# Kernel optimization log

Hardware: AMD Instinct MI355X
Metric: run time of the kernel (lower is better)

The kernel has to match this reference:

```python
import jax, jax.numpy as jnp
import numpy as np

N_NODES = 100000
N_EDGES = 1600000
MAX_RADIUS = 3.0
NUM_BASIS = 3
SQRT2 = 2.0 ** 0.5
# e3nn soft_one_hot_linspace 'smooth_finite' prefactor
C_SMOOTH = 1.14136 * float(np.exp(2.0))


def _sus(x):
    # smooth unit step: exp(-1/x) for x>0 else 0 (NaN-safe for grad)
    safe = jnp.where(x > 0.0, x, 1.0)
    return jnp.where(x > 0.0, jnp.exp(-1.0 / safe), 0.0)


def radial_embed(d):
    # soft_one_hot_linspace(d, 0, max_radius, 3, basis='smooth_finite', cutoff=True) * sqrt(num_basis)
    values = jnp.linspace(0.0, MAX_RADIUS, NUM_BASIS + 2)[1:-1]  # [3]
    step = MAX_RADIUS / (NUM_BASIS + 1)
    diff = (d[:, None] - values) / step  # [E,3]
    y = C_SMOOTH * _sus(diff + 1.0) * _sus(1.0 - diff)
    return y * (NUM_BASIS ** 0.5)


def fcnet(x, w1, w2):
    # e3nn FullyConnectedNet([3,16,numel], relu): normalized weights, normalize2mom(relu)=sqrt(2)*relu
    h = SQRT2 * jax.nn.relu(x @ (w1 / w1.shape[0] ** 0.5))
    return h @ (w2 / w2.shape[0] ** 0.5)


def reference(pos, feat, edge_src, edge_dst, fc1_w1, fc1_w2, core_w1, core_w2, fc3_w1, fc3_w2, conv_w, conv_b):
    n = pos.shape[0]
    z = edge_src.shape[0] / n  # average num neighbors
    edge_vec = pos[edge_dst] - pos[edge_src]
    d = jnp.sqrt(jnp.sum(edge_vec * edge_vec, axis=1))  # edges are self-loop-free -> d > 0
    emb = radial_embed(d)  # [E,3]

    # NOTE on e3nn math: with input/mid/output parities all even and sh = 0e+1o+2e,
    # the only parity-allowed paths producing nonzero output are the 0e (scalar) paths,
    # which contract against Y_0 = 1 ('component' normalization). The 4x1e block of the
    # mid irreps is identically zero (no parity-allowed path ever populates it), so the
    # math below (scalar block only, with e3nn path weights) is exactly equivalent.
    def conv(x, w1, w2, mul_in, mul_out, path_w):
        # per-edge weights from radial MLP; keep the 0e->0e instruction block
        w = fcnet(emb, w1, w2)[:, : mul_in * mul_out].reshape(-1, mul_in, mul_out)
        msg = path_w * jnp.einsum('euw,eu->ew', w, x[edge_src])
        return jax.ops.segment_sum(msg, edge_dst, num_segments=n) / z ** 0.5

    x = conv(feat, fc1_w1, fc1_w2, 3, 4, (1.0 / 3.0) ** 0.5)  # tp1: fan_in 3*1 -> pw=1/sqrt(3)
    for i in range(3):
        x = conv(x, core_w1[i], core_w2[i], 4, 4, 0.5)  # tp2 0e path: pw=sqrt(1/4)
    x = conv(x, fc3_w1, fc3_w2, 4, 16, 0.5)  # tp3: pw=sqrt(1/4)
    # Conv1d(16, 2, 1) == pointwise linear
    return x @ conv_w.T + conv_b


def setup_inputs():
    key = jax.random.key(0)
    ks = jax.random.split(key, 12)
    pos = jax.random.uniform(ks[0], (N_NODES, 3), dtype=jnp.float32)  # unit box -> all edge lengths < max_radius
    feat = jax.random.normal(ks[1], (N_NODES, 3), dtype=jnp.float32)
    edge_src = jax.random.randint(ks[2], (N_EDGES,), 0, N_NODES, dtype=jnp.int32)
    off = jax.random.randint(ks[3], (N_EDGES,), 1, N_NODES, dtype=jnp.int32)
    edge_dst = ((edge_src + off) % N_NODES).astype(jnp.int32)  # radius_graph has no self-loops
    return {
        'pos': pos,
        'feat': feat,
        'edge_src': edge_src,
        'edge_dst': edge_dst,
        'fc1_w1': jax.random.normal(ks[4], (3, 16), jnp.float32),
        'fc1_w2': jax.random.normal(ks[5], (16, 12), jnp.float32),
        'core_w1': jax.random.normal(ks[6], (3, 3, 16), jnp.float32),
        'core_w2': jax.random.normal(ks[7], (3, 16, 48), jnp.float32),
        'fc3_w1': jax.random.normal(ks[8], (3, 16), jnp.float32),
        'fc3_w2': jax.random.normal(ks[9], (16, 64), jnp.float32),
        'conv_w': jax.random.normal(ks[10], (2, 16), jnp.float32) * 0.25,
        'conv_b': jax.random.normal(ks[11], (2,), jnp.float32) * 0.1,
    }
```

## Files before the change

### kernel.cpp

```cpp
#include <hip/hip_runtime.h>


#define BCAP 4608
#define NBMAX 400

__device__ __forceinline__ float sus_f(float x) {
    return x > 0.0f ? __expf(-1.0f / x) : 0.0f;
}

__device__ __forceinline__ float uload(const float* p) {
    return __uint_as_float(__builtin_amdgcn_readfirstlane(__float_as_uint(*p)));
}

__global__ __launch_bounds__(128) void k_prep_g(
    const float* __restrict__ w2, const float* __restrict__ cw,
    float* __restrict__ gbuf)
{
    int idx = threadIdx.x;
    int k = idx >> 3, u = (idx >> 1) & 3, c = idx & 1;
    float s = 0.0f;
    #pragma unroll
    for (int w = 0; w < 16; ++w)
        s = fmaf(w2[k * 64 + u * 16 + w], cw[c * 16 + w], s);
    gbuf[idx] = s;
}

__global__ __launch_bounds__(256) void k_bin(
    const int* __restrict__ src, const int* __restrict__ dst,
    int* __restrict__ gcur, int* __restrict__ ptmp,
    int nedges, int nb)
{
    __shared__ int cnt[NBMAX];
    __shared__ int gb[NBMAX];
    for (int b = threadIdx.x; b < nb; b += 256) cnt[b] = 0;
    __syncthreads();

    int base = blockIdx.x * 2048 + threadIdx.x * 8;
    int pk[8]; int bk[8]; short r[8];
    int ss[8], dd[8];
    if (base + 7 < nedges) {
        int4 s0 = *(const int4*)&src[base];
        int4 s1 = *(const int4*)&src[base + 4];
        int4 d0 = *(const int4*)&dst[base];
        int4 d1 = *(const int4*)&dst[base + 4];
        ss[0]=s0.x; ss[1]=s0.y; ss[2]=s0.z; ss[3]=s0.w;
        ss[4]=s1.x; ss[5]=s1.y; ss[6]=s1.z; ss[7]=s1.w;
        dd[0]=d0.x; dd[1]=d0.y; dd[2]=d0.z; dd[3]=d0.w;
        dd[4]=d1.x; dd[5]=d1.y; dd[6]=d1.z; dd[7]=d1.w;
        #pragma unroll
        for (int i = 0; i < 8; ++i) {
            int b = dd[i] >> 8;
            bk[i] = b;
            pk[i] = (ss[i] << 8) | (dd[i] & 255);
            r[i] = (short)atomicAdd(&cnt[b], 1);
        }
    } else {
        #pragma unroll
        for (int i = 0; i < 8; ++i) {
            int e = base + i;
            if (e < nedges) {
                int s = src[e], t = dst[e];
                int b = t >> 8;
                bk[i] = b;
                pk[i] = (s << 8) | (t & 255);
                r[i] = (short)atomicAdd(&cnt[b], 1);
            } else bk[i] = -1;
        }
    }
    __syncthreads();
    for (int b = threadIdx.x; b < nb; b += 256) {
        int c = cnt[b];
        gb[b] = c > 0 ? atomicAdd(&gcur[b], c) : 0;
    }
    __syncthreads();
    #pragma unroll
    for (int i = 0; i < 8; ++i) {
        if (bk[i] >= 0) {
            int p = gb[bk[i]] + (int)r[i];
            if (p < BCAP)
                ptmp[bk[i] * BCAP + p] = pk[i];
        }
    }
}

__global__ __launch_bounds__(256) void k_build(
    const int* __restrict__ gcur, const int* __restrict__ ptmp,
    int* __restrict__ pidx, int2* __restrict__ offs2,
    int n, int nb)
{
    int b = blockIdx.x;
    int cnt = gcur[b]; if (cnt > BCAP) cnt = BCAP;

    __shared__ int stage[BCAP];
    __shared__ int perm[BCAP];
    __shared__ int deg[256];
    __shared__ int loffs[256];
    __shared__ int cur[256];

    const int* tin = ptmp + b * BCAP;
    for (int j = threadIdx.x; j < cnt; j += 256) stage[j] = tin[j];
    deg[threadIdx.x] = 0;
    __syncthreads();

    for (int j = threadIdx.x; j < cnt; j += 256)
        atomicAdd(&deg[stage[j] & 255], 1);
    __syncthreads();

    {
        int t = threadIdx.x;
        int v = deg[t];
        loffs[t] = v; __syncthreads();
        for (int off = 1; off < 256; off <<= 1) {
            int val = (t >= off) ? loffs[t - off] : 0;
            __syncthreads();
            loffs[t] += val;
            __syncthreads();
        }
        int incl = loffs[t];
        __syncthreads();
        loffs[t] = incl - v;
        cur[t] = incl - v;
        __syncthreads();
    }

    {
        int nid0 = b << 8;
        int nn = n - nid0; if (nn > 256) nn = 256;
        int t = threadIdx.x;
        if (t < nn) {
            int st = b * BCAP + loffs[t];
            offs2[nid0 + t] = make_int2(st, st + deg[t]);
        }
    }

    for (int j = threadIdx.x; j < cnt; j += 256) {
        int pkd = stage[j];
        perm[atomicAdd(&cur[pkd & 255], 1)] = pkd;
    }
    __syncthreads();

    int* tout = pidx + b * BCAP;
    for (int j = threadIdx.x; j < cnt; j += 256) tout[j] = perm[j];
}

__global__ __launch_bounds__(256) void k_emb(
    const float* __restrict__ pos, const int* __restrict__ gcur,
    const int* __restrict__ pidx, float4* __restrict__ ebuf)
{
    int b = blockIdx.y;
    int j = blockIdx.x * 256 + threadIdx.x;
    if (j >= gcur[b]) return;
    int pkd = pidx[b * BCAP + j];
    int s = pkd >> 8;
    int t = (b << 8) | (pkd & 255);
    float dx = pos[3 * t + 0] - pos[3 * s + 0];
    float dy = pos[3 * t + 1] - pos[3 * s + 1];
    float dz = pos[3 * t + 2] - pos[3 * s + 2];
    float d = sqrtf(dx * dx + dy * dy + dz * dz);
    const float C = 1.14136f * 7.3890560989306495f;
    float e0, e1, e2;
    { float f = (d - 0.75f) * (1.0f / 0.75f);
      e0 = C * sus_f(f + 1.0f) * sus_f(1.0f - f); }
    { float f = (d - 1.50f) * (1.0f / 0.75f);
      e1 = C * sus_f(f + 1.0f) * sus_f(1.0f - f); }
    { float f = (d - 2.25f) * (1.0f / 0.75f);
      e2 = C * sus_f(f + 1.0f) * sus_f(1.0f - f); }
    ebuf[(size_t)b * BCAP + j] = make_float4(__int_as_float(s), e0, e1, e2);
}


__global__ __launch_bounds__(256) void k_node_l1(
    const float* __restrict__ feat, const float4* __restrict__ edata,
    const int2* __restrict__ offs2,
    const float* __restrict__ w1, const float* __restrict__ w2,
    float* __restrict__ xout, int n)
{
    __shared__ float lw[16 * 20];
    if (threadIdx.x < 192) {
        int k = threadIdx.x / 12, r = threadIdx.x % 12;
        lw[k * 20 + r] = w2[k * 12 + r];
    }
    __syncthreads();

    int g = blockIdx.x * 256 + threadIdx.x;
    int nd = g >> 2;
    if (nd >= n) return;
    int t = g & 3;

    float w1r[3][16];
    #pragma unroll
    for (int j = 0; j < 3; ++j)
        #pragma unroll
        for (int k = 0; k < 16; ++k) w1r[j][k] = uload(&w1[j * 16 + k]);

    float O[16][3];
    #pragma unroll
    for (int k = 0; k < 16; ++k)
        #pragma unroll
        for (int u = 0; u < 3; ++u) O[k][u] = 0.0f;

    int2 se = offs2[nd];
    for (int e = se.x + t; e < se.y; e += 4) {
        float4 ed = edata[e];
        int s = __float_as_int(ed.x);
        float f0 = feat[3 * s + 0], f1 = feat[3 * s + 1], f2 = feat[3 * s + 2];
        #pragma unroll
        for (int k = 0; k < 16; ++k) {
            float a = fmaf(ed.y, w1r[0][k], fmaf(ed.z, w1r[1][k], ed.w * w1r[2][k]));
            float h = a > 0.0f ? a : 0.0f;
            O[k][0] = fmaf(h, f0, O[k][0]);
            O[k][1] = fmaf(h, f1, O[k][1]);
            O[k][2] = fmaf(h, f2, O[k][2]);
        }
    }

    float p0 = 0.f, p1 = 0.f, p2 = 0.f, p3 = 0.f;
    #pragma unroll
    for (int k = 0; k < 16; ++k)
        #pragma unroll
        for (int u = 0; u < 3; ++u) {
            const float4 q = *(const float4*)&lw[k * 20 + u * 4];
            float o = O[k][u];
            p0 = fmaf(o, q.x, p0); p1 = fmaf(o, q.y, p1);
            p2 = fmaf(o, q.z, p2); p3 = fmaf(o, q.w, p3);
        }
    p0 += __shfl_xor(p0, 1); p1 += __shfl_xor(p1, 1);
    p2 += __shfl_xor(p2, 1); p3 += __shfl_xor(p3, 1);
    p0 += __shfl_xor(p0, 2); p1 += __shfl_xor(p1, 2);
    p2 += __shfl_xor(p2, 2); p3 += __shfl_xor(p3, 2);
    if (t == 0) {
        const float S = 0.051031036307982884f;
        float4 o; o.x = p0 * S; o.y = p1 * S; o.z = p2 * S; o.w = p3 * S;
        ((float4*)xout)[nd] = o;
    }
}

__global__ __launch_bounds__(256) void k_node_core(
    const float4* __restrict__ xin, const float4* __restrict__ edata,
    const int2* __restrict__ offs2,
    const float* __restrict__ w1, const float* __restrict__ w2,
    float* __restrict__ xout, int n)
{
    __shared__ float lw[16 * 20];
    {
        int idx = threadIdx.x;
        int k = idx >> 4, r = idx & 15;
        lw[k * 20 + r] = w2[k * 48 + r];
    }
    __syncthreads();

    int g = blockIdx.x * 256 + threadIdx.x;
    int nd = g >> 2;
    if (nd >= n) return;
    int t = g & 3;

    float w1r[3][16];
    #pragma unroll
    for (int j = 0; j < 3; ++j)
        #pragma unroll
        for (int k = 0; k < 16; ++k) w1r[j][k] = uload(&w1[j * 16 + k]);

    float O[16][4];
    #pragma unroll
    for (int k = 0; k < 16; ++k)
        #pragma unroll
        for (int u = 0; u < 4; ++u) O[k][u] = 0.0f;

    int2 se = offs2[nd];
    for (int e = se.x + t; e < se.y; e += 4) {
        float4 ed = edata[e];
        int s = __float_as_int(ed.x);
        float4 x = xin[s];
        #pragma unroll
        for (int k = 0; k < 16; ++k) {
            float a = fmaf(ed.y, w1r[0][k], fmaf(ed.z, w1r[1][k], ed.w * w1r[2][k]));
            float h = a > 0.0f ? a : 0.0f;
            O[k][0] = fmaf(h, x.x, O[k][0]);
            O[k][1] = fmaf(h, x.y, O[k][1]);
            O[k][2] = fmaf(h, x.z, O[k][2]);
            O[k][3] = fmaf(h, x.w, O[k][3]);
        }
    }

    float p0 = 0.f, p1 = 0.f, p2 = 0.f, p3 = 0.f;
    #pragma unroll
    for (int k = 0; k < 16; ++k)
        #pragma unroll
        for (int u = 0; u < 4; ++u) {
            const float4 q = *(const float4*)&lw[k * 20 + u * 4];
            float o = O[k][u];
            p0 = fmaf(o, q.x, p0); p1 = fmaf(o, q.y, p1);
            p2 = fmaf(o, q.z, p2); p3 = fmaf(o, q.w, p3);
        }
    p0 += __shfl_xor(p0, 1); p1 += __shfl_xor(p1, 1);
    p2 += __shfl_xor(p2, 1); p3 += __shfl_xor(p3, 1);
    p0 += __shfl_xor(p0, 2); p1 += __shfl_xor(p1, 2);
    p2 += __shfl_xor(p2, 2); p3 += __shfl_xor(p3, 2);
    if (t == 0) {
        const float S = 0.04419417382415922f;
        float4 o; o.x = p0 * S; o.y = p1 * S; o.z = p2 * S; o.w = p3 * S;
        ((float4*)xout)[nd] = o;
    }
}

__global__ __launch_bounds__(256) void k_node_fc3_final(
    const float4* __restrict__ xin, const float4* __restrict__ edata,
    const int2* __restrict__ offs2,
    const float* __restrict__ w1, const float* __restrict__ gbuf,
    const float* __restrict__ cb,
    float* __restrict__ out, int n)
{
    __shared__ float lg[128];
    if (threadIdx.x < 128) lg[threadIdx.x] = gbuf[threadIdx.x];
    __syncthreads();

    int g = blockIdx.x * 256 + threadIdx.x;
    int nd = g >> 2;
    if (nd >= n) return;
    int t = g & 3;

    float w1r[3][16];
    #pragma unroll
    for (int j = 0; j < 3; ++j)
        #pragma unroll
        for (int k = 0; k < 16; ++k) w1r[j][k] = uload(&w1[j * 16 + k]);

    float O[16][4];
    #pragma unroll
    for (int k = 0; k < 16; ++k)
        #pragma unroll
        for (int u = 0; u < 4; ++u) O[k][u] = 0.0f;

    int2 se = offs2[nd];
    for (int e = se.x + t; e < se.y; e += 4) {
        float4 ed = edata[e];
        int s = __float_as_int(ed.x);
        float4 x = xin[s];
        #pragma unroll
        for (int k = 0; k < 16; ++k) {
            float a = fmaf(ed.y, w1r[0][k], fmaf(ed.z, w1r[1][k], ed.w * w1r[2][k]));
            float h = a > 0.0f ? a : 0.0f;
            O[k][0] = fmaf(h, x.x, O[k][0]);
            O[k][1] = fmaf(h, x.y, O[k][1]);
            O[k][2] = fmaf(h, x.z, O[k][2]);
            O[k][3] = fmaf(h, x.w, O[k][3]);
        }
    }

    float a0 = 0.f, a1 = 0.f;
    #pragma unroll
    for (int k = 0; k < 16; ++k)
        #pragma unroll
        for (int u = 0; u < 4; ++u) {
            float o = O[k][u];
            const float2 q = *(const float2*)&lg[(k * 4 + u) * 2];
            a0 = fmaf(o, q.x, a0);
            a1 = fmaf(o, q.y, a1);
        }
    a0 += __shfl_xor(a0, 1); a1 += __shfl_xor(a1, 1);
    a0 += __shfl_xor(a0, 2); a1 += __shfl_xor(a1, 2);
    if (t == 0) {
        const float S = 0.04419417382415922f;
        float2 o; o.x = fmaf(a0, S, cb[0]); o.y = fmaf(a1, S, cb[1]);
        ((float2*)out)[nd] = o;
    }
}


extern "C" void kernel_launch(void* const* d_in, const int* in_sizes, int n_in,
                              void* d_out, int out_size, void* d_ws, size_t ws_size,
                              hipStream_t stream) {
    const float* pos     = (const float*)d_in[0];
    const float* feat    = (const float*)d_in[1];
    const int*   esrc    = (const int*)d_in[2];
    const int*   edst    = (const int*)d_in[3];
    const float* fc1_w1  = (const float*)d_in[4];
    const float* fc1_w2  = (const float*)d_in[5];
    const float* core_w1 = (const float*)d_in[6];
    const float* core_w2 = (const float*)d_in[7];
    const float* fc3_w1  = (const float*)d_in[8];
    const float* fc3_w2  = (const float*)d_in[9];
    const float* conv_w  = (const float*)d_in[10];
    const float* conv_b  = (const float*)d_in[11];
    float* out = (float*)d_out;

    const int E = in_sizes[2];
    const int N = in_sizes[0] / 3;
    const int nb = (N + 255) >> 8;

    float4* ebuf = (float4*)d_ws;
    int* ptmp  = (int*)(ebuf + (size_t)nb * BCAP);
    int* pidx  = ptmp + (size_t)nb * BCAP;
    float* xa  = (float*)(pidx + (size_t)nb * BCAP);
    float* xb  = xa + (size_t)4 * N;
    int2* offs2 = (int2*)(xb + (size_t)4 * N);
    int* gcur  = (int*)(offs2 + N);
    float* gbuf = (float*)(gcur + ((nb + 3) & ~3));

    int g4 = (4 * N + 255) / 256;

    hipMemsetAsync(gcur, 0, (size_t)nb * sizeof(int), stream);
    k_prep_g<<<1, 128, 0, stream>>>(fc3_w2, conv_w, gbuf);
    k_bin<<<(E + 2047) / 2048, 256, 0, stream>>>(esrc, edst, gcur, ptmp, E, nb);
    k_build<<<nb, 256, 0, stream>>>(gcur, ptmp, pidx, offs2, N, nb);
    {
        dim3 eg(BCAP / 256, nb);
        k_emb<<<eg, 256, 0, stream>>>(pos, gcur, pidx, ebuf);
    }

    k_node_l1<<<g4, 256, 0, stream>>>(feat, ebuf, offs2, fc1_w1, fc1_w2, xa, N);
    k_node_core<<<g4, 256, 0, stream>>>((const float4*)xa, ebuf, offs2,
                                        core_w1 + 0, core_w2 + 0, xb, N);
    k_node_core<<<g4, 256, 0, stream>>>((const float4*)xb, ebuf, offs2,
                                        core_w1 + 48, core_w2 + 768, xa, N);
    k_node_core<<<g4, 256, 0, stream>>>((const float4*)xa, ebuf, offs2,
                                        core_w1 + 96, core_w2 + 1536, xb, N);
    k_node_fc3_final<<<g4, 256, 0, stream>>>((const float4*)xb, ebuf, offs2,
                                             fc3_w1, gbuf, conv_b, out, N);
}
```

Baseline: 240.2 us.

## Split hidden units across node threads instead of edges to cut register pressure

```diff
diff --git a/kernel.cpp b/kernel.cpp
--- a/kernel.cpp
+++ b/kernel.cpp
@@ -6,10 +6,6 @@
 
 __device__ __forceinline__ float sus_f(float x) {
     return x > 0.0f ? __expf(-1.0f / x) : 0.0f;
-}
-
-__device__ __forceinline__ float uload(const float* p) {
-    return __uint_as_float(__builtin_amdgcn_readfirstlane(__float_as_uint(*p)));
 }
 
 __global__ __launch_bounds__(128) void k_prep_g(
@@ -187,40 +183,67 @@
     if (nd >= n) return;
     int t = g & 3;
 
-    float w1r[3][16];
+    float w1r[3][4];
     #pragma unroll
     for (int j = 0; j < 3; ++j)
         #pragma unroll
-        for (int k = 0; k < 16; ++k) w1r[j][k] = uload(&w1[j * 16 + k]);
-
-    float O[16][3];
-    #pragma unroll
-    for (int k = 0; k < 16; ++k)
-        #pragma unroll
-        for (int u = 0; u < 3; ++u) O[k][u] = 0.0f;
+        for (int kk = 0; kk < 4; ++kk) w1r[j][kk] = w1[j * 16 + 4 * t + kk];
+
+    float O[4][3];
+    #pragma unroll
+    for (int kk = 0; kk < 4; ++kk)
+        #pragma unroll
+        for (int u = 0; u < 3; ++u) O[kk][u] = 0.0f;
 
     int2 se = offs2[nd];
-    for (int e = se.x + t; e < se.y; e += 4) {
+    int e = se.x;
+    for (; e + 4 <= se.y; e += 4) {
+        float4 ed0 = edata[e], ed1 = edata[e + 1],
+               ed2 = edata[e + 2], ed3 = edata[e + 3];
+        int s0 = __float_as_int(ed0.x), s1 = __float_as_int(ed1.x),
+            s2 = __float_as_int(ed2.x), s3 = __float_as_int(ed3.x);
+        float f00 = feat[3*s0], f01 = feat[3*s0+1], f02 = feat[3*s0+2];
+        float f10 = feat[3*s1], f11 = feat[3*s1+1], f12 = feat[3*s1+2];
+        float f20 = feat[3*s2], f21 = feat[3*s2+1], f22 = feat[3*s2+2];
+        float f30 = feat[3*s3], f31 = feat[3*s3+1], f32 = feat[3*s3+2];
+        #pragma unroll
+        for (int kk = 0; kk < 4; ++kk) {
+            float a, h;
+            a = fmaf(ed0.y, w1r[0][kk], fmaf(ed0.z, w1r[1][kk], ed0.w * w1r[2][kk]));
+            h = a > 0.0f ? a : 0.0f;
+            O[kk][0] = fmaf(h, f00, O[kk][0]); O[kk][1] = fmaf(h, f01, O[kk][1]); O[kk][2] = fmaf(h, f02, O[kk][2]);
+            a = fmaf(ed1.y, w1r[0][kk], fmaf(ed1.z, w1r[1][kk], ed1.w * w1r[2][kk]));
+            h = a > 0.0f ? a : 0.0f;
+            O[kk][0] = fmaf(h, f10, O[kk][0]); O[kk][1] = fmaf(h, f11, O[kk][1]); O[kk][2] = fmaf(h, f12, O[kk][2]);
+            a = fmaf(ed2.y, w1r[0][kk], fmaf(ed2.z, w1r[1][kk], ed2.w * w1r[2][kk]));
+            h = a > 0.0f ? a : 0.0f;
+            O[kk][0] = fmaf(h, f20, O[kk][0]); O[kk][1] = fmaf(h, f21, O[kk][1]); O[kk][2] = fmaf(h, f22, O[kk][2]);
+            a = fmaf(ed3.y, w1r[0][kk], fmaf(ed3.z, w1r[1][kk], ed3.w * w1r[2][kk]));
+            h = a > 0.0f ? a : 0.0f;
+            O[kk][0] = fmaf(h, f30, O[kk][0]); O[kk][1] = fmaf(h, f31, O[kk][1]); O[kk][2] = fmaf(h, f32, O[kk][2]);
+        }
+    }
+    for (; e < se.y; ++e) {
         float4 ed = edata[e];
         int s = __float_as_int(ed.x);
-        float f0 = feat[3 * s + 0], f1 = feat[3 * s + 1], f2 = feat[3 * s + 2];
-        #pragma unroll
-        for (int k = 0; k < 16; ++k) {
-            float a = fmaf(ed.y, w1r[0][k], fmaf(ed.z, w1r[1][k], ed.w * w1r[2][k]));
+        float f0 = feat[3*s], f1 = feat[3*s+1], f2 = feat[3*s+2];
+        #pragma unroll
+        for (int kk = 0; kk < 4; ++kk) {
+            float a = fmaf(ed.y, w1r[0][kk], fmaf(ed.z, w1r[1][kk], ed.w * w1r[2][kk]));
             float h = a > 0.0f ? a : 0.0f;
-            O[k][0] = fmaf(h, f0, O[k][0]);
-            O[k][1] = fmaf(h, f1, O[k][1]);
-            O[k][2] = fmaf(h, f2, O[k][2]);
+            O[kk][0] = fmaf(h, f0, O[kk][0]);
+            O[kk][1] = fmaf(h, f1, O[kk][1]);
+            O[kk][2] = fmaf(h, f2, O[kk][2]);
         }
     }
 
     float p0 = 0.f, p1 = 0.f, p2 = 0.f, p3 = 0.f;
     #pragma unroll
-    for (int k = 0; k < 16; ++k)
+    for (int kk = 0; kk < 4; ++kk)
         #pragma unroll
         for (int u = 0; u < 3; ++u) {
-            const float4 q = *(const float4*)&lw[k * 20 + u * 4];
-            float o = O[k][u];
+            const float4 q = *(const float4*)&lw[(4 * t + kk) * 20 + u * 4];
+            float o = O[kk][u];
             p0 = fmaf(o, q.x, p0); p1 = fmaf(o, q.y, p1);
             p2 = fmaf(o, q.z, p2); p3 = fmaf(o, q.w, p3);
         }
@@ -254,41 +277,67 @@
     if (nd >= n) return;
     int t = g & 3;
 
-    float w1r[3][16];
+    float w1r[3][4];
     #pragma unroll
     for (int j = 0; j < 3; ++j)
         #pragma unroll
-        for (int k = 0; k < 16; ++k) w1r[j][k] = uload(&w1[j * 16 + k]);
-
-    float O[16][4];
-    #pragma unroll
-    for (int k = 0; k < 16; ++k)
-        #pragma unroll
-        for (int u = 0; u < 4; ++u) O[k][u] = 0.0f;
+        for (int kk = 0; kk < 4; ++kk) w1r[j][kk] = w1[j * 16 + 4 * t + kk];
+
+    float O[4][4];
+    #pragma unroll
+    for (int kk = 0; kk < 4; ++kk)
+        #pragma unroll
+        for (int u = 0; u < 4; ++u) O[kk][u] = 0.0f;
 
     int2 se = offs2[nd];
-    for (int e = se.x + t; e < se.y; e += 4) {
+    int e = se.x;
+    for (; e + 4 <= se.y; e += 4) {
+        float4 ed0 = edata[e], ed1 = edata[e + 1],
+               ed2 = edata[e + 2], ed3 = edata[e + 3];
+        float4 x0 = xin[__float_as_int(ed0.x)];
+        float4 x1 = xin[__float_as_int(ed1.x)];
+        float4 x2 = xin[__float_as_int(ed2.x)];
+        float4 x3 = xin[__float_as_int(ed3.x)];
+        #pragma unroll
+        for (int kk = 0; kk < 4; ++kk) {
+            float a, h;
+            a = fmaf(ed0.y, w1r[0][kk], fmaf(ed0.z, w1r[1][kk], ed0.w * w1r[2][kk]));
+            h = a > 0.0f ? a : 0.0f;
+            O[kk][0] = fmaf(h, x0.x, O[kk][0]); O[kk][1] = fmaf(h, x0.y, O[kk][1]);
+            O[kk][2] = fmaf(h, x0.z, O[kk][2]); O[kk][3] = fmaf(h, x0.w, O[kk][3]);
+            a = fmaf(ed1.y, w1r[0][kk], fmaf(ed1.z, w1r[1][kk], ed1.w * w1r[2][kk]));
+            h = a > 0.0f ? a : 0.0f;
+            O[kk][0] = fmaf(h, x1.x, O[kk][0]); O[kk][1] = fmaf(h, x1.y, O[kk][1]);
+            O[kk][2] = fmaf(h, x1.z, O[kk][2]); O[kk][3] = fmaf(h, x1.w, O[kk][3]);
+            a = fmaf(ed2.y, w1r[0][kk], fmaf(ed2.z, w1r[1][kk], ed2.w * w1r[2][kk]));
+            h = a > 0.0f ? a : 0.0f;
+            O[kk][0] = fmaf(h, x2.x, O[kk][0]); O[kk][1] = fmaf(h, x2.y, O[kk][1]);
+            O[kk][2] = fmaf(h, x2.z, O[kk][2]); O[kk][3] = fmaf(h, x2.w, O[kk][3]);
+            a = fmaf(ed3.y, w1r[0][kk], fmaf(ed3.z, w1r[1][kk], ed3.w * w1r[2][kk]));
+            h = a > 0.0f ? a : 0.0f;
+            O[kk][0] = fmaf(h, x3.x, O[kk][0]); O[kk][1] = fmaf(h, x3.y, O[kk][1]);
+            O[kk][2] = fmaf(h, x3.z, O[kk][2]); O[kk][3] = fmaf(h, x3.w, O[kk][3]);
+        }
+    }
+    for (; e < se.y; ++e) {
         float4 ed = edata[e];
-        int s = __float_as_int(ed.x);
-        float4 x = xin[s];
-        #pragma unroll
-        for (int k = 0; k < 16; ++k) {
-            float a = fmaf(ed.y, w1r[0][k], fmaf(ed.z, w1r[1][k], ed.w * w1r[2][k]));
+        float4 x = xin[__float_as_int(ed.x)];
+        #pragma unroll
+        for (int kk = 0; kk < 4; ++kk) {
+            float a = fmaf(ed.y, w1r[0][kk], fmaf(ed.z, w1r[1][kk], ed.w * w1r[2][kk]));
             float h = a > 0.0f ? a : 0.0f;
-            O[k][0] = fmaf(h, x.x, O[k][0]);
-            O[k][1] = fmaf(h, x.y, O[k][1]);
-            O[k][2] = fmaf(h, x.z, O[k][2]);
-            O[k][3] = fmaf(h, x.w, O[k][3]);
+            O[kk][0] = fmaf(h, x.x, O[kk][0]); O[kk][1] = fmaf(h, x.y, O[kk][1]);
+            O[kk][2] = fmaf(h, x.z, O[kk][2]); O[kk][3] = fmaf(h, x.w, O[kk][3]);
         }
     }
 
     float p0 = 0.f, p1 = 0.f, p2 = 0.f, p3 = 0.f;
     #pragma unroll
-    for (int k = 0; k < 16; ++k)
+    for (int kk = 0; kk < 4; ++kk)
         #pragma unroll
         for (int u = 0; u < 4; ++u) {
-            const float4 q = *(const float4*)&lw[k * 20 + u * 4];
-            float o = O[k][u];
+            const float4 q = *(const float4*)&lw[(4 * t + kk) * 20 + u * 4];
+            float o = O[kk][u];
             p0 = fmaf(o, q.x, p0); p1 = fmaf(o, q.y, p1);
             p2 = fmaf(o, q.z, p2); p3 = fmaf(o, q.w, p3);
         }
@@ -319,41 +368,67 @@
     if (nd >= n) return;
     int t = g & 3;
 
-    float w1r[3][16];
+    float w1r[3][4];
     #pragma unroll
     for (int j = 0; j < 3; ++j)
         #pragma unroll
-        for (int k = 0; k < 16; ++k) w1r[j][k] = uload(&w1[j * 16 + k]);
-
-    float O[16][4];
-    #pragma unroll
-    for (int k = 0; k < 16; ++k)
-        #pragma unroll
-        for (int u = 0; u < 4; ++u) O[k][u] = 0.0f;
+        for (int kk = 0; kk < 4; ++kk) w1r[j][kk] = w1[j * 16 + 4 * t + kk];
+
+    float O[4][4];
+    #pragma unroll
+    for (int kk = 0; kk < 4; ++kk)
+        #pragma unroll
+        for (int u = 0; u < 4; ++u) O[kk][u] = 0.0f;
 
     int2 se = offs2[nd];
-    for (int e = se.x + t; e < se.y; e += 4) {
+    int e = se.x;
+    for (; e + 4 <= se.y; e += 4) {
+        float4 ed0 = edata[e], ed1 = edata[e + 1],
+               ed2 = edata[e + 2], ed3 = edata[e + 3];
+        float4 x0 = xin[__float_as_int(ed0.x)];
+        float4 x1 = xin[__float_as_int(ed1.x)];
+        float4 x2 = xin[__float_as_int(ed2.x)];
+        float4 x3 = xin[__float_as_int(ed3.x)];
+        #pragma unroll
+        for (int kk = 0; kk < 4; ++kk) {
+            float a, h;
+            a = fmaf(ed0.y, w1r[0][kk], fmaf(ed0.z, w1r[1][kk], ed0.w * w1r[2][kk]));
+            h = a > 0.0f ? a : 0.0f;
+            O[kk][0] = fmaf(h, x0.x, O[kk][0]); O[kk][1] = fmaf(h, x0.y, O[kk][1]);
+            O[kk][2] = fmaf(h, x0.z, O[kk][2]); O[kk][3] = fmaf(h, x0.w, O[kk][3]);
+            a = fmaf(ed1.y, w1r[0][kk], fmaf(ed1.z, w1r[1][kk], ed1.w * w1r[2][kk]));
+            h = a > 0.0f ? a : 0.0f;
+            O[kk][0] = fmaf(h, x1.x, O[kk][0]); O[kk][1] = fmaf(h, x1.y, O[kk][1]);
+            O[kk][2] = fmaf(h, x1.z, O[kk][2]); O[kk][3] = fmaf(h, x1.w, O[kk][3]);
+            a = fmaf(ed2.y, w1r[0][kk], fmaf(ed2.z, w1r[1][kk], ed2.w * w1r[2][kk]));
+            h = a > 0.0f ? a : 0.0f;
+            O[kk][0] = fmaf(h, x2.x, O[kk][0]); O[kk][1] = fmaf(h, x2.y, O[kk][1]);
+            O[kk][2] = fmaf(h, x2.z, O[kk][2]); O[kk][3] = fmaf(h, x2.w, O[kk][3]);
+            a = fmaf(ed3.y, w1r[0][kk], fmaf(ed3.z, w1r[1][kk], ed3.w * w1r[2][kk]));
+            h = a > 0.0f ? a : 0.0f;
+            O[kk][0] = fmaf(h, x3.x, O[kk][0]); O[kk][1] = fmaf(h, x3.y, O[kk][1]);
+            O[kk][2] = fmaf(h, x3.z, O[kk][2]); O[kk][3] = fmaf(h, x3.w, O[kk][3]);
+        }
+    }
+    for (; e < se.y; ++e) {
         float4 ed = edata[e];
-        int s = __float_as_int(ed.x);
-        float4 x = xin[s];
-        #pragma unroll
-        for (int k = 0; k < 16; ++k) {
-            float a = fmaf(ed.y, w1r[0][k], fmaf(ed.z, w1r[1][k], ed.w * w1r[2][k]));
+        float4 x = xin[__float_as_int(ed.x)];
+        #pragma unroll
+        for (int kk = 0; kk < 4; ++kk) {
+            float a = fmaf(ed.y, w1r[0][kk], fmaf(ed.z, w1r[1][kk], ed.w * w1r[2][kk]));
             float h = a > 0.0f ? a : 0.0f;
-            O[k][0] = fmaf(h, x.x, O[k][0]);
-            O[k][1] = fmaf(h, x.y, O[k][1]);
-            O[k][2] = fmaf(h, x.z, O[k][2]);
-            O[k][3] = fmaf(h, x.w, O[k][3]);
+            O[kk][0] = fmaf(h, x.x, O[kk][0]); O[kk][1] = fmaf(h, x.y, O[kk][1]);
+            O[kk][2] = fmaf(h, x.z, O[kk][2]); O[kk][3] = fmaf(h, x.w, O[kk][3]);
         }
     }
 
     float a0 = 0.f, a1 = 0.f;
     #pragma unroll
-    for (int k = 0; k < 16; ++k)
+    for (int kk = 0; kk < 4; ++kk)
         #pragma unroll
         for (int u = 0; u < 4; ++u) {
-            float o = O[k][u];
-            const float2 q = *(const float2*)&lg[(k * 4 + u) * 2];
+            float o = O[kk][u];
+            const float2 q = *(const float2*)&lg[(((4 * t + kk) * 4) + u) * 2];
             a0 = fmaf(o, q.x, a0);
             a1 = fmaf(o, q.y, a1);
         }
```

Result: no change. 243.3 us (+1.3%).
